# Optimization experiments

Hardware: AMD Instinct MI355X
Metric: run time of the kernel (lower is better)

Reference implementation:

```python
import jax, jax.numpy as jnp
import numpy as np

B, L, V, D, H, DK, NL, M = 4, 1024, 64, 256, 4, 64, 4, 20
FF = 4 * D
EPS = 1e-5


def _rel_table(seq_len, m):
    # abs(i-j), log-bucketed beyond m, clipped to [0, 2m] -> int indices [L, L]
    d = jnp.abs(jnp.arange(seq_len)[:, None] - jnp.arange(seq_len)[None, :]).astype(jnp.float32)
    d = jnp.where(d > m, m + jnp.log2(jnp.maximum(d - m, 1.0)), d)
    return jnp.clip(d, 0, 2 * m).astype(jnp.int32)


def _layer_norm(x, g, b):
    mu = jnp.mean(x, axis=-1, keepdims=True)
    var = jnp.mean(jnp.square(x - mu), axis=-1, keepdims=True)
    return (x - mu) * jax.lax.rsqrt(var + EPS) * g + b


def setup_inputs() -> dict:
    key = jax.random.key(0)
    ks = jax.random.split(key, 16)
    w = lambda i, shape: jax.random.normal(ks[i], shape, jnp.float32) * 0.05
    return {
        "x": jax.random.normal(ks[0], (B, L, V), jnp.float32),
        "emb": w(1, (V, D)),
        "Wq": w(2, (NL, D, H * DK)), "bq": jnp.zeros((NL, H * DK), jnp.float32),
        "Wk": w(3, (NL, D, H * DK)), "bk": jnp.zeros((NL, H * DK), jnp.float32),
        "Wv": w(4, (NL, D, H * DK)), "bv": jnp.zeros((NL, H * DK), jnp.float32),
        "Wo": w(5, (NL, H * DK, D)), "bo": jnp.zeros((NL, D), jnp.float32),
        "rel_k": 1.0 + w(6, (NL, 2 * M + 1, H)),  # multiplicative bias ~1
        "rel_b": w(7, (NL, 2 * M + 1, H)),
        "ln1_g": jnp.ones((NL, D), jnp.float32), "ln1_b": jnp.zeros((NL, D), jnp.float32),
        "W1": w(8, (NL, D, FF)), "b1": jnp.zeros((NL, FF), jnp.float32),
        "W2": w(9, (NL, FF, D)), "b2": jnp.zeros((NL, D), jnp.float32),
        "ln2_g": jnp.ones((NL, D), jnp.float32), "ln2_b": jnp.zeros((NL, D), jnp.float32),
    }


def reference(x, emb, Wq, bq, Wk, bk, Wv, bv, Wo, bo, rel_k, rel_b,
              ln1_g, ln1_b, W1, b1, W2, b2, ln2_g, ln2_b):
    h = x @ emb  # [B, L, D]  (dropout inactive: eval mode)
    table = _rel_table(L, M)  # [L, L] int32
    inv_sqrt_dk = jnp.float32(1.0 / np.sqrt(DK))
    attns = []
    for l in range(NL):
        q = (h @ Wq[l] + bq[l]).reshape(B, L, H, DK)
        k = (h @ Wk[l] + bk[l]).reshape(B, L, H, DK)
        v = (h @ Wv[l] + bv[l]).reshape(B, L, H, DK)
        scores = jnp.einsum('blhk,bmhk->bhlm', q, k) * inv_sqrt_dk
        # per-head relative-position bias (table symmetric, so axis order of L,L is immaterial)
        bias_k = jnp.transpose(rel_k[l][table], (2, 1, 0))  # [H, L, L]
        bias_b = jnp.transpose(rel_b[l][table], (2, 1, 0))  # [H, L, L]
        scores = scores * bias_k[None] + bias_b[None]
        attn = jax.nn.softmax(scores, axis=-1)  # attn dropout inactive (eval)
        attns.append(attn)
        out = jnp.einsum('bhlm,bmhk->blhk', attn, v).reshape(B, L, H * DK) @ Wo[l] + bo[l]
        # FeedForwardNetwork (note: source has NO residual connections)
        y = _layer_norm(out, ln1_g[l], ln1_b[l])
        y = jax.nn.gelu(y @ W1[l] + b1[l], approximate=False) @ W2[l] + b2[l]
        h = _layer_norm(y, ln2_g[l], ln2_b[l])
    avg_attn = jnp.mean(jnp.stack(attns, axis=0), axis=0)  # [B, H, L, L]
    return h.mean(axis=1), avg_attn
```

## Files before the change

kernel.cpp:

```cpp
#include <hip/hip_runtime.h>
#include <hip/hip_bf16.h>
#include <math.h>

#define Bn 4
#define Ln 1024
#define Vn 64
#define Dn 256
#define Hn 4
#define DKn 64
#define NLn 4
#define Mn 20
#define FFn 1024
#define NTOK (Bn * Ln)
#define QKVW 768
#define LOG2E 1.4426950408889634f
#define PELEMS (Bn * Hn * Ln * Ln)

typedef __attribute__((ext_vector_type(8))) short bf16x8;
typedef __attribute__((ext_vector_type(4))) float f32x4;

__device__ __forceinline__ ushort f2b(float f) {
    uint u = __float_as_uint(f);
    u += 0x7fff + ((u >> 16) & 1);
    return (ushort)(u >> 16);
}
__device__ __forceinline__ float b2f(ushort u) {
    return __uint_as_float(((uint)u) << 16);
}

__global__ __launch_bounds__(256) void embed_k(const float* __restrict__ X,
                                               const float* __restrict__ E,
                                               ushort* __restrict__ Hb) {
    __shared__ float xs[Vn];
    int n = blockIdx.x, d = threadIdx.x;
    if (threadIdx.x < Vn) xs[threadIdx.x] = X[n * Vn + threadIdx.x];
    __syncthreads();
    float s = 0.f;
#pragma unroll
    for (int v = 0; v < Vn; ++v) s += xs[v] * E[v * Dn + d];
    Hb[(size_t)n * Dn + d] = f2b(s);
}

__global__ __launch_bounds__(256) void relbias_k(const float* __restrict__ rk,
                                                 const float* __restrict__ rb,
                                                 float* __restrict__ bkT,
                                                 float* __restrict__ bbT) {
    int tid = blockIdx.x * 256 + threadIdx.x;
    int dist = tid & 1023;
    int hh = (tid >> 10) & 3;
    int l = tid >> 12;
    float dd = (float)dist;
    if (dist > Mn) dd = (float)Mn + log2f((float)(dist - Mn));
    if (dd > 2.0f * Mn) dd = 2.0f * Mn;
    int idx = (int)dd;
    bkT[tid] = rk[(l * (2 * Mn + 1) + idx) * Hn + hh] * 0.125f * LOG2E;
    bbT[tid] = rb[(l * (2 * Mn + 1) + idx) * Hn + hh] * LOG2E;
}

__global__ __launch_bounds__(256) void prep_bias(const float* __restrict__ bq,
                                                 const float* __restrict__ bk,
                                                 const float* __restrict__ bv,
                                                 float* __restrict__ bqkv) {
    int idx = blockIdx.x * 256 + threadIdx.x;
    int l = idx / QKVW, r = idx - l * QKVW;
    float v;
    if (r < 256)      v = bq[l * 256 + r];
    else if (r < 512) v = bk[l * 256 + r - 256];
    else              v = bv[l * 256 + r - 512];
    bqkv[idx] = v;
}

__global__ __launch_bounds__(256) void transpose_cvt(
    const float* __restrict__ src, ushort* __restrict__ dst,
    int R, int C, int srcLS, int dstLS) {
    __shared__ float s[32][33];
    src += (size_t)blockIdx.z * srcLS;
    dst += (size_t)blockIdx.z * dstLS;
    int r0 = blockIdx.y * 32, c0 = blockIdx.x * 32;
    int tx = threadIdx.x & 31, ty = threadIdx.x >> 5;
#pragma unroll
    for (int ii = 0; ii < 4; ++ii)
        s[ty + 8 * ii][tx] = src[(size_t)(r0 + ty + 8 * ii) * C + c0 + tx];
    __syncthreads();
#pragma unroll
    for (int ii = 0; ii < 4; ++ii)
        dst[(size_t)(c0 + ty + 8 * ii) * R + r0 + tx] = f2b(s[tx][ty + 8 * ii]);
}

#define GST 72
#define GEMM_KK_MFMA(KK)                                                      \
    {                                                                         \
        bf16x8 a0 = *(const bf16x8*)&As[(wm * 32 + l15) * GST + (KK)*32 + lg * 8];      \
        bf16x8 a1 = *(const bf16x8*)&As[(wm * 32 + 16 + l15) * GST + (KK)*32 + lg * 8]; \
        bf16x8 b0 = *(const bf16x8*)&Bs[(wn * 32 + l15) * GST + (KK)*32 + lg * 8];      \
        bf16x8 b1 = *(const bf16x8*)&Bs[(wn * 32 + 16 + l15) * GST + (KK)*32 + lg * 8]; \
        acc[0][0] = __builtin_amdgcn_mfma_f32_16x16x32_bf16(a0, b0, acc[0][0], 0, 0, 0); \
        acc[0][1] = __builtin_amdgcn_mfma_f32_16x16x32_bf16(a0, b1, acc[0][1], 0, 0, 0); \
        acc[1][0] = __builtin_amdgcn_mfma_f32_16x16x32_bf16(a1, b0, acc[1][0], 0, 0, 0); \
        acc[1][1] = __builtin_amdgcn_mfma_f32_16x16x32_bf16(a1, b1, acc[1][1], 0, 0, 0); \
    }

template <int LNA>
__global__ __launch_bounds__(256) void gemm_mfma(
    const ushort* __restrict__ A, const ushort* __restrict__ Bt,
    const float* __restrict__ bias, ushort* __restrict__ C,
    int M, int N, int K, int act,
    const float* __restrict__ lng, const float* __restrict__ lnb,
    ushort* __restrict__ Vt_out) {
    __shared__ __align__(16) ushort As[64 * GST];
    __shared__ __align__(16) ushort Bs[64 * GST];
    __shared__ float gl[256];
    __shared__ float bl[256];
    int t = threadIdx.x;
    int lane = t & 63, w = t >> 6;
    int wm = w >> 1, wn = w & 1;
    int l15 = lane & 15, lg = lane >> 4;
    int mBase = blockIdx.y * 64, nBase = blockIdx.x * 64;
    int lrow = t >> 2, lkc = (t & 3) * 16;
    const ushort* Ap = A + (size_t)(mBase + lrow) * K + lkc;
    const ushort* Bp = Bt + (size_t)(nBase + lrow) * K + lkc;
    f32x4 acc[2][2] = {};

    if constexpr (LNA) {
        uint4 areg[8];
        float s = 0.f;
#pragma unroll
        for (int kc = 0; kc < 4; ++kc)
#pragma unroll
            for (int h = 0; h < 2; ++h) {
                areg[kc * 2 + h] = *(const uint4*)(Ap + kc * 64 + h * 8);
                const ushort* e = (const ushort*)&areg[kc * 2 + h];
#pragma unroll
                for (int q = 0; q < 8; ++q) s += b2f(e[q]);
            }
        s += __shfl_xor(s, 1, 64);
        s += __shfl_xor(s, 2, 64);
        float mu = s * (1.0f / 256.0f);
        float vv = 0.f;
#pragma unroll
        for (int kc = 0; kc < 8; ++kc) {
            const ushort* e = (const ushort*)&areg[kc];
#pragma unroll
            for (int q = 0; q < 8; ++q) {
                float d = b2f(e[q]) - mu;
                vv += d * d;
            }
        }
        vv += __shfl_xor(vv, 1, 64);
        vv += __shfl_xor(vv, 2, 64);
        float rs = rsqrtf(vv * (1.0f / 256.0f) + 1e-5f);
        gl[t] = lng[t];
        bl[t] = lnb[t];
        __syncthreads();
#pragma unroll
        for (int kc = 0; kc < 4; ++kc) {
            uint4 bv0 = *(const uint4*)(Bp + kc * 64);
            uint4 bv1 = *(const uint4*)(Bp + kc * 64 + 8);
            __syncthreads();
#pragma unroll
            for (int h = 0; h < 2; ++h) {
                const ushort* e = (const ushort*)&areg[kc * 2 + h];
                ushort outv[8];
#pragma unroll
                for (int q = 0; q < 8; ++q) {
                    int col = kc * 64 + lkc + h * 8 + q;
                    outv[q] = f2b((b2f(e[q]) - mu) * rs * gl[col] + bl[col]);
                }
                *(uint4*)&As[lrow * GST + lkc + h * 8] = *(const uint4*)outv;
            }
            *(uint4*)&Bs[lrow * GST + lkc] = bv0;
            *(uint4*)&Bs[lrow * GST + lkc + 8] = bv1;
            __syncthreads();
            GEMM_KK_MFMA(0)
            GEMM_KK_MFMA(1)
        }
    } else {
        for (int k0 = 0; k0 < K; k0 += 64) {
            uint4 av0 = *(const uint4*)(Ap + k0);
            uint4 av1 = *(const uint4*)(Ap + k0 + 8);
            uint4 bv0 = *(const uint4*)(Bp + k0);
            uint4 bv1 = *(const uint4*)(Bp + k0 + 8);
            __syncthreads();
            *(uint4*)&As[lrow * GST + lkc] = av0;
            *(uint4*)&As[lrow * GST + lkc + 8] = av1;
            *(uint4*)&Bs[lrow * GST + lkc] = bv0;
            *(uint4*)&Bs[lrow * GST + lkc + 8] = bv1;
            __syncthreads();
            GEMM_KK_MFMA(0)
            GEMM_KK_MFMA(1)
        }
    }
    if (Vt_out != nullptr && nBase >= 512) {
#pragma unroll
        for (int ni = 0; ni < 2; ++ni) {
            int col = nBase + wn * 32 + ni * 16 + l15;
            float bc = bias[col];
            int d = col - 512;
#pragma unroll
            for (int mi = 0; mi < 2; ++mi) {
                int rb = mBase + wm * 32 + mi * 16 + lg * 4;
                int bb_ = rb >> 10, i_ = rb & 1023;
                size_t vb = ((size_t)(bb_ * 4 + (d >> 6)) * 64 + (d & 63)) * Ln + i_;
                ushort o4[4];
#pragma unroll
                for (int j = 0; j < 4; ++j) o4[j] = f2b(acc[mi][ni][j] + bc);
                *(ushort4*)&Vt_out[vb] = *(const ushort4*)o4;
            }
        }
        return;
    }
#pragma unroll
    for (int ni = 0; ni < 2; ++ni) {
        int col = nBase + wn * 32 + ni * 16 + l15;
        float bc = bias[col];
#pragma unroll
        for (int mi = 0; mi < 2; ++mi) {
            int rb = mBase + wm * 32 + mi * 16 + lg * 4;
#pragma unroll
            for (int j = 0; j < 4; ++j) {
                float v = acc[mi][ni][j] + bc;
                if (act) v = v * 0.5f * (1.0f + erff(v * 0.7071067811865475f));
                C[(size_t)(rb + j) * N + col] = f2b(v);
            }
        }
    }
}

#define G2ST 72
template <int LNA, int SPLITK>
__global__ __launch_bounds__(512) void gemm128(
    const ushort* __restrict__ A, const ushort* __restrict__ Bt,
    const float* __restrict__ bias, ushort* __restrict__ C,
    float* __restrict__ Cpart,
    int M, int N, int K, int act,
    const float* __restrict__ lng, const float* __restrict__ lnb,
    ushort* __restrict__ Vt_out) {
    __shared__ __align__(16) ushort As[128 * G2ST];
    __shared__ __align__(16) ushort Bs[128 * G2ST];
    __shared__ float gl[256];
    __shared__ float bl[256];
    int t = threadIdx.x;
    int lane = t & 63, w = t >> 6;
    int wm = w >> 2, wn = w & 3;
    int l15 = lane & 15, lg = lane >> 4;
    int mBase = blockIdx.y * 128, nBase = blockIdx.x * 128;
    int srow = t >> 2, skof = (t & 3) * 16;
    int kbeg = (SPLITK > 1) ? blockIdx.z * 256 : 0;
    const ushort* Ap = A + (size_t)(mBase + srow) * K + kbeg + skof;
    const ushort* Bp = Bt + (size_t)(nBase + srow) * K + kbeg + skof;
    f32x4 acc[4][2] = {};

    float mu = 0.f, rs = 0.f;
    uint4 areg[8];
    if constexpr (LNA) {
        float s = 0.f;
#pragma unroll
        for (int kc = 0; kc < 4; ++kc)
#pragma unroll
            for (int h = 0; h < 2; ++h) {
                areg[kc * 2 + h] = *(const uint4*)(Ap + kc * 64 + h * 8);
                const ushort* e = (const ushort*)&areg[kc * 2 + h];
#pragma unroll
                for (int z = 0; z < 8; ++z) s += b2f(e[z]);
            }
        s += __shfl_xor(s, 1, 64);
        s += __shfl_xor(s, 2, 64);
        mu = s * (1.0f / 256.0f);
        float vv = 0.f;
#pragma unroll
        for (int q = 0; q < 8; ++q) {
            const ushort* e = (const ushort*)&areg[q];
#pragma unroll
            for (int z = 0; z < 8; ++z) {
                float d = b2f(e[z]) - mu;
                vv += d * d;
            }
        }
        vv += __shfl_xor(vv, 1, 64);
        vv += __shfl_xor(vv, 2, 64);
        rs = rsqrtf(vv * (1.0f / 256.0f) + 1e-5f);
        if (t < 256) {
            gl[t] = lng[t];
            bl[t] = lnb[t];
        }
    }

#pragma unroll
    for (int kc = 0; kc < 4; ++kc) {
        uint4 av0, av1, bv0, bv1;
        if constexpr (!LNA) {
            av0 = *(const uint4*)(Ap + kc * 64);
            av1 = *(const uint4*)(Ap + kc * 64 + 8);
        }
        bv0 = *(const uint4*)(Bp + kc * 64);
        bv1 = *(const uint4*)(Bp + kc * 64 + 8);
        __syncthreads();
        if constexpr (LNA) {
#pragma unroll
            for (int h = 0; h < 2; ++h) {
                const ushort* e = (const ushort*)&areg[kc * 2 + h];
                ushort outv[8];
#pragma unroll
                for (int z = 0; z < 8; ++z) {
                    int col = kc * 64 + skof + h * 8 + z;
                    outv[z] = f2b((b2f(e[z]) - mu) * rs * gl[col] + bl[col]);
                }
                *(uint4*)&As[srow * G2ST + skof + h * 8] = *(const uint4*)outv;
            }
        } else {
            *(uint4*)&As[srow * G2ST + skof] = av0;
            *(uint4*)&As[srow * G2ST + skof + 8] = av1;
        }
        *(uint4*)&Bs[srow * G2ST + skof] = bv0;
        *(uint4*)&Bs[srow * G2ST + skof + 8] = bv1;
        __syncthreads();
#pragma unroll
        for (int kk = 0; kk < 2; ++kk) {
            bf16x8 af[4], bfr[2];
#pragma unroll
            for (int mi = 0; mi < 4; ++mi)
                af[mi] = *(const bf16x8*)&As[(wm * 64 + mi * 16 + l15) * G2ST + kk * 32 + lg * 8];
#pragma unroll
            for (int ni = 0; ni < 2; ++ni)
                bfr[ni] = *(const bf16x8*)&Bs[(wn * 32 + ni * 16 + l15) * G2ST + kk * 32 + lg * 8];
#pragma unroll
            for (int mi = 0; mi < 4; ++mi)
#pragma unroll
                for (int ni = 0; ni < 2; ++ni)
                    acc[mi][ni] = __builtin_amdgcn_mfma_f32_16x16x32_bf16(
                        af[mi], bfr[ni], acc[mi][ni], 0, 0, 0);
        }
    }

    if (Vt_out != nullptr && nBase >= 512) {
#pragma unroll
        for (int ni = 0; ni < 2; ++ni) {
            int col = nBase + wn * 32 + ni * 16 + l15;
            float bc = bias[col];
            int d = col - 512;
#pragma unroll
            for (int mi = 0; mi < 4; ++mi) {
                int rb = mBase + wm * 64 + mi * 16 + lg * 4;
                int bb_ = rb >> 10, i_ = rb & 1023;
                size_t vb = ((size_t)(bb_ * 4 + (d >> 6)) * 64 + (d & 63)) * Ln + i_;
                ushort o4[4];
#pragma unroll
                for (int j = 0; j < 4; ++j) o4[j] = f2b(acc[mi][ni][j] + bc);
                *(ushort4*)&Vt_out[vb] = *(const ushort4*)o4;
            }
        }
        return;
    }
    if constexpr (SPLITK > 1) {
#pragma unroll
        for (int ni = 0; ni < 2; ++ni) {
            int col = nBase + wn * 32 + ni * 16 + l15;
#pragma unroll
            for (int mi = 0; mi < 4; ++mi) {
                int rb = mBase + wm * 64 + mi * 16 + lg * 4;
#pragma unroll
                for (int j = 0; j < 4; ++j)
                    Cpart[((size_t)blockIdx.z * M + rb + j) * N + col] = acc[mi][ni][j];
            }
        }
        return;
    }
#pragma unroll
    for (int ni = 0; ni < 2; ++ni) {
        int col = nBase + wn * 32 + ni * 16 + l15;
        float bc = bias[col];
#pragma unroll
        for (int mi = 0; mi < 4; ++mi) {
            int rb = mBase + wm * 64 + mi * 16 + lg * 4;
#pragma unroll
            for (int j = 0; j < 4; ++j) {
                float v = acc[mi][ni][j] + bc;
                if (act) v = v * 0.5f * (1.0f + erff(v * 0.7071067811865475f));
                C[(size_t)(rb + j) * N + col] = f2b(v);
            }
        }
    }
}

__global__ __launch_bounds__(256) void combine_k(const float* __restrict__ part,
                                                 const float* __restrict__ bias,
                                                 ushort* __restrict__ C) {
    size_t e = ((size_t)blockIdx.x * 256 + threadIdx.x) * 4;
    const size_t MN = (size_t)NTOK * Dn;
    float4 s = *(const float4*)&bias[(int)(e & 255)];
#pragma unroll
    for (int z = 0; z < 4; ++z) {
        float4 p = *(const float4*)&part[z * MN + e];
        s.x += p.x; s.y += p.y; s.z += p.z; s.w += p.w;
    }
    ushort4 o;
    o.x = f2b(s.x); o.y = f2b(s.y); o.z = f2b(s.z); o.w = f2b(s.w);
    *(ushort4*)&C[e] = o;
}

#define PWST 40
#define NW 8
template <int MODE>
__global__ __launch_bounds__(512) void attn_fused(
    const ushort* __restrict__ qkv, const ushort* __restrict__ Vt,
    const float* __restrict__ bkTab, const float* __restrict__ bbTab,
    ushort* __restrict__ ctx, float* __restrict__ avg,
    ushort* __restrict__ Pout, int first) {
    __shared__ float bk_l[Ln];
    __shared__ float bb_l[Ln];
    __shared__ __align__(16) char uni[20480];
    __shared__ float mm[NW][16];
    __shared__ float ll[NW][16];

    int t = threadIdx.x;
    int lane = t & 63, w = t >> 6;
    int wn = w & 3, wc = w >> 2;
    int l15 = lane & 15, lg = lane >> 4;

    ushort* pwh = (ushort*)&uni[w * 2560];
    ushort* pwl = (ushort*)&uni[w * 2560 + 1280];

    int bid = blockIdx.x;
    int xcd = bid & 7, sub = bid >> 3;
    int bh = xcd * 2 + (sub >> 6);
    int q = sub & 63;
    int b = bh >> 2, hh = bh & 3;
    int i0 = q * 16;

#pragma unroll
    for (int ii = 0; ii < 2; ++ii) {
        bk_l[t + 512 * ii] = bkTab[hh * Ln + t + 512 * ii];
        bb_l[t + 512 * ii] = bbTab[hh * Ln + t + 512 * ii];
    }
    __syncthreads();

    bf16x8 qa0, qa1;
    {
        const ushort* qp = qkv + (size_t)(b * Ln + i0 + l15) * QKVW + hh * DKn;
        qa0 = *(const bf16x8*)(qp + lg * 8);
        qa1 = *(const bf16x8*)(qp + 32 + lg * 8);
    }

    const ushort* kbase = qkv + (size_t)(b * Ln) * QKVW + Dn + hh * DKn;

    f32x4 sv[8];
    float m[4] = {-1e30f, -1e30f, -1e30f, -1e30f};
#pragma unroll
    for (int cl = 0; cl < 8; ++cl) {
        int c = wc * 8 + cl;
        const ushort* kp = kbase + (size_t)(c * 64 + wn * 16 + l15) * QKVW;
        bf16x8 k0 = *(const bf16x8*)(kp + lg * 8);
        bf16x8 k1 = *(const bf16x8*)(kp + 32 + lg * 8);
        f32x4 acc = {};
        acc = __builtin_amdgcn_mfma_f32_16x16x32_bf16(qa0, k0, acc, 0, 0, 0);
        acc = __builtin_amdgcn_mfma_f32_16x16x32_bf16(qa1, k1, acc, 0, 0, 0);
        int j = c * 64 + wn * 16 + l15;
#pragma unroll
        for (int r = 0; r < 4; ++r) {
            int i = i0 + lg * 4 + r;
            int dist = (i > j) ? (i - j) : (j - i);
            float s = acc[r] * bk_l[dist] + bb_l[dist];
            sv[cl][r] = s;
            m[r] = fmaxf(m[r], s);
        }
    }
#pragma unroll
    for (int mask = 1; mask < 16; mask <<= 1)
#pragma unroll
        for (int r = 0; r < 4; ++r) m[r] = fmaxf(m[r], __shfl_xor(m[r], mask, 64));
    if (l15 == 0)
#pragma unroll
        for (int r = 0; r < 4; ++r) mm[w][lg * 4 + r] = m[r];
    __syncthreads();
#pragma unroll
    for (int r = 0; r < 4; ++r) {
        int row = lg * 4 + r;
        float m0 = fmaxf(fmaxf(mm[0][row], mm[1][row]), fmaxf(mm[2][row], mm[3][row]));
        float m1 = fmaxf(fmaxf(mm[4][row], mm[5][row]), fmaxf(mm[6][row], mm[7][row]));
        m[r] = fmaxf(m0, m1);
    }
    float lsum[4] = {0.f, 0.f, 0.f, 0.f};
#pragma unroll
    for (int cl = 0; cl < 8; ++cl)
#pragma unroll
        for (int r = 0; r < 4; ++r) {
            float p = exp2f(sv[cl][r] - m[r]);
            sv[cl][r] = p;
            lsum[r] += p;
        }
#pragma unroll
    for (int mask = 1; mask < 16; mask <<= 1)
#pragma unroll
        for (int r = 0; r < 4; ++r) lsum[r] += __shfl_xor(lsum[r], mask, 64);
    if (l15 == 0)
#pragma unroll
        for (int r = 0; r < 4; ++r) ll[w][lg * 4 + r] = lsum[r];
    __syncthreads();
    float invl[4];
#pragma unroll
    for (int r = 0; r < 4; ++r) {
        int row = lg * 4 + r;
        invl[r] = 1.0f / (ll[0][row] + ll[1][row] + ll[2][row] + ll[3][row] +
                          ll[4][row] + ll[5][row] + ll[6][row] + ll[7][row]);
    }

    const ushort* vbase = Vt + (size_t)bh * DKn * Ln;
    float* avgrow = avg + ((size_t)bh * Ln + i0) * Ln;
    int iw = lane >> 2, jq = lane & 3;
    f32x4 acco[4] = {};
#pragma unroll
    for (int p = 0; p < 4; ++p) {
        const int c0 = wc * 8 + 2 * p, c1 = c0 + 1;
        float aold[2][4];
        if (MODE == 0 && !first) {
#pragma unroll
            for (int cc = 0; cc < 2; ++cc)
#pragma unroll
                for (int r = 0; r < 4; ++r)
                    aold[cc][r] = avgrow[(size_t)(lg * 4 + r) * Ln +
                                         (c0 + cc) * 64 + wn * 16 + l15];
        }
#pragma unroll
        for (int cc = 0; cc < 2; ++cc)
#pragma unroll
            for (int r = 0; r < 4; ++r) {
                float pv = sv[2 * p + cc][r] * invl[r];
                sv[2 * p + cc][r] = pv;
                ushort ph = f2b(pv);
                int off = (lg * 4 + r) * PWST + cc * 16 + l15;
                pwh[off] = ph;
                pwl[off] = f2b(pv - b2f(ph));
            }
        int kcol = (lg < 2 ? c0 : c1) * 64 + wn * 16 + (lg & 1) * 8;
        bf16x8 va0 = *(const bf16x8*)(vbase + (size_t)(0 * 16 + l15) * Ln + kcol);
        bf16x8 va1 = *(const bf16x8*)(vbase + (size_t)(1 * 16 + l15) * Ln + kcol);
        bf16x8 va2 = *(const bf16x8*)(vbase + (size_t)(2 * 16 + l15) * Ln + kcol);
        bf16x8 va3 = *(const bf16x8*)(vbase + (size_t)(3 * 16 + l15) * Ln + kcol);
        bf16x8 pbh = *(const bf16x8*)&pwh[l15 * PWST + lg * 8];
        bf16x8 pbl = *(const bf16x8*)&pwl[l15 * PWST + lg * 8];
        acco[0] = __builtin_amdgcn_mfma_f32_16x16x32_bf16(va0, pbh, acco[0], 0, 0, 0);
        acco[1] = __builtin_amdgcn_mfma_f32_16x16x32_bf16(va1, pbh, acco[1], 0, 0, 0);
        acco[2] = __builtin_amdgcn_mfma_f32_16x16x32_bf16(va2, pbh, acco[2], 0, 0, 0);
        acco[3] = __builtin_amdgcn_mfma_f32_16x16x32_bf16(va3, pbh, acco[3], 0, 0, 0);
        acco[0] = __builtin_amdgcn_mfma_f32_16x16x32_bf16(va0, pbl, acco[0], 0, 0, 0);
        acco[1] = __builtin_amdgcn_mfma_f32_16x16x32_bf16(va1, pbl, acco[1], 0, 0, 0);
        acco[2] = __builtin_amdgcn_mfma_f32_16x16x32_bf16(va2, pbl, acco[2], 0, 0, 0);
        acco[3] = __builtin_amdgcn_mfma_f32_16x16x32_bf16(va3, pbl, acco[3], 0, 0, 0);
        if (MODE == 0) {
#pragma unroll
            for (int cc = 0; cc < 2; ++cc)
#pragma unroll
                for (int r = 0; r < 4; ++r) {
                    float v = 0.25f * sv[2 * p + cc][r];
                    if (!first) v += aold[cc][r];
                    avgrow[(size_t)(lg * 4 + r) * Ln + (c0 + cc) * 64 + wn * 16 + l15] = v;
                }
        } else if (MODE == 1) {
            size_t tb = ((((size_t)bid * 8 + w) * 4 + p) * 2) * 256 + (size_t)lane * 4;
            ushort4 ph0 = *(const ushort4*)&pwh[iw * PWST + 0 * 16 + jq * 4];
            ushort4 ph1 = *(const ushort4*)&pwh[iw * PWST + 1 * 16 + jq * 4];
            *(ushort4*)&Pout[tb] = ph0;
            *(ushort4*)&Pout[tb + 256] = ph1;
        } else {
#pragma unroll
            for (int cc = 0; cc < 2; ++cc) {
                int c = c0 + cc;
                size_t tb = ((((size_t)bid * 8 + w) * 4 + p) * 2 + cc) * 256 +
                            (size_t)lane * 4;
                ushort4 p0 = *(const ushort4*)&Pout[tb];
                ushort4 p1 = *(const ushort4*)&Pout[(size_t)PELEMS + tb];
                ushort4 p2 = *(const ushort4*)&Pout[(size_t)2 * PELEMS + tb];
                ushort4 p3 = *(const ushort4*)&pwh[iw * PWST + cc * 16 + jq * 4];
                const ushort* q0 = (const ushort*)&p0;
                const ushort* q1 = (const ushort*)&p1;
                const ushort* q2 = (const ushort*)&p2;
                const ushort* q3 = (const ushort*)&p3;
                size_t base = ((size_t)(bh * Ln) + i0 + iw) * Ln +
                              c * 64 + wn * 16 + jq * 4;
                float4 o;
                float* op_ = (float*)&o;
#pragma unroll
                for (int k = 0; k < 4; ++k)
                    op_[k] = 0.25f * (b2f(q0[k]) + b2f(q1[k]) + b2f(q2[k]) + b2f(q3[k]));
                *(float4*)&avg[base] = o;
            }
        }
    }

    __syncthreads();
    {
        float* op = (float*)&uni[wn * 4096];
        if (wc == 1) {
#pragma unroll
            for (int dg = 0; dg < 4; ++dg)
#pragma unroll
                for (int r = 0; r < 4; ++r)
                    op[(dg * 16 + lg * 4 + r) * 16 + l15] = acco[dg][r];
        }
    }
    __syncthreads();
    {
        float* op = (float*)&uni[wn * 4096];
        if (wc == 0) {
#pragma unroll
            for (int dg = 0; dg < 4; ++dg)
#pragma unroll
                for (int r = 0; r < 4; ++r)
                    op[(dg * 16 + lg * 4 + r) * 16 + l15] += acco[dg][r];
        }
    }
    __syncthreads();
#pragma unroll
    for (int k = 0; k < 2; ++k) {
        int idx = t + 512 * k;
        float v = ((const float*)&uni[0])[idx] + ((const float*)&uni[4096])[idx] +
                  ((const float*)&uni[8192])[idx] + ((const float*)&uni[12288])[idx];
        int dd = idx >> 4, ii = idx & 15;
        ctx[(size_t)(b * Ln + i0 + ii) * Dn + hh * DKn + dd] = f2b(v);
    }
}

__global__ __launch_bounds__(256) void layernorm_k(const ushort* __restrict__ X,
                                                   const float* __restrict__ g,
                                                   const float* __restrict__ bta,
                                                   ushort* __restrict__ Y) {
    int w = threadIdx.x >> 6, lane = threadIdx.x & 63;
    int row = blockIdx.x * 4 + w;
    const ushort* xr = X + (size_t)row * Dn;
    float x[4];
#pragma unroll
    for (int ii = 0; ii < 4; ++ii) x[ii] = b2f(xr[lane + 64 * ii]);
    float s = x[0] + x[1] + x[2] + x[3];
#pragma unroll
    for (int m = 1; m < 64; m <<= 1) s += __shfl_xor(s, m, 64);
    float mu = s * (1.0f / 256.0f);
    float vs = 0.f;
#pragma unroll
    for (int ii = 0; ii < 4; ++ii) {
        float d = x[ii] - mu;
        vs += d * d;
    }
#pragma unroll
    for (int m = 1; m < 64; m <<= 1) vs += __shfl_xor(vs, m, 64);
    float rs = rsqrtf(vs * (1.0f / 256.0f) + 1e-5f);
#pragma unroll
    for (int ii = 0; ii < 4; ++ii) {
        int d = lane + 64 * ii;
        Y[(size_t)row * Dn + d] = f2b((x[ii] - mu) * rs * g[d] + bta[d]);
    }
}

__global__ __launch_bounds__(256) void mean_part_k(const ushort* __restrict__ Hb,
                                                   float* __restrict__ part) {
    int blk = blockIdx.x;
    int b = blk >> 4, g = blk & 15;
    int d = threadIdx.x;
    float s = 0.f;
#pragma unroll
    for (int r = 0; r < 64; ++r)
        s += b2f(Hb[(size_t)(b * Ln + g * 64 + r) * Dn + d]);
    part[(size_t)blk * Dn + d] = s;
}
__global__ __launch_bounds__(256) void mean_final_k(const float* __restrict__ part,
                                                    float* __restrict__ out) {
    int b = blockIdx.x, d = threadIdx.x;
    float s = 0.f;
#pragma unroll
    for (int g = 0; g < 16; ++g) s += part[(size_t)(b * 16 + g) * Dn + d];
    out[b * Dn + d] = s * (1.0f / (float)Ln);
}

extern "C" void kernel_launch(void* const* d_in, const int* in_sizes, int n_in,
                              void* d_out, int out_size, void* d_ws, size_t ws_size,
                              hipStream_t stream) {
    const float* x    = (const float*)d_in[0];
    const float* emb  = (const float*)d_in[1];
    const float* Wq   = (const float*)d_in[2];
    const float* bq   = (const float*)d_in[3];
    const float* Wk   = (const float*)d_in[4];
    const float* bk   = (const float*)d_in[5];
    const float* Wv   = (const float*)d_in[6];
    const float* bv   = (const float*)d_in[7];
    const float* Wo   = (const float*)d_in[8];
    const float* bo   = (const float*)d_in[9];
    const float* rk   = (const float*)d_in[10];
    const float* rb   = (const float*)d_in[11];
    const float* ln1g = (const float*)d_in[12];
    const float* ln1b = (const float*)d_in[13];
    const float* W1   = (const float*)d_in[14];
    const float* b1   = (const float*)d_in[15];
    const float* W2   = (const float*)d_in[16];
    const float* b2   = (const float*)d_in[17];
    const float* ln2g = (const float*)d_in[18];
    const float* ln2b = (const float*)d_in[19];

    float* out = (float*)d_out;
    float* avg = out + Bn * Dn;

    char* ws = (char*)d_ws;
    const size_t MB = 1024 * 1024;
    ushort* hb   = (ushort*)(ws);
    ushort* qkvb = (ushort*)(ws + 2 * MB);
    ushort* ctxb = (ushort*)(ws + 8 * MB);
    ushort* t1   = (ushort*)(ws + 10 * MB);
    ushort* ffb  = (ushort*)(ws + 12 * MB);
    ushort* qkvT = (ushort*)(ws + 20 * MB);
    ushort* WoT  = (ushort*)(ws + 22 * MB);
    ushort* W1T  = (ushort*)(ws + 23 * MB);
    ushort* W2T  = (ushort*)(ws + 25 * MB);
    float*  bqkv = (float*)(ws + 27 * MB);
    float*  bkT  = (float*)(ws + 27 * MB + 65536);
    float*  bbT  = (float*)(ws + 27 * MB + 131072);
    ushort* Vt   = (ushort*)(ws + 30 * MB);
    float*  mpart= (float*)(ws + 33 * MB);
    ushort* Pbuf = (ushort*)(ws + 36 * MB);
    float*  fpart= (float*)(ws + 132 * MB);

    const size_t need = 132 * MB + (size_t)4 * NTOK * Dn * sizeof(float);
    const bool fancy = (ws_size >= need);

    embed_k<<<NTOK, 256, 0, stream>>>(x, emb, hb);
    relbias_k<<<64, 256, 0, stream>>>(rk, rb, bkT, bbT);
    prep_bias<<<12, 256, 0, stream>>>(bq, bk, bv, bqkv);

    dim3 t88(8, 8, NLn);
    transpose_cvt<<<t88, 256, 0, stream>>>(Wq, qkvT + 0,      256, 256, 65536, 196608);
    transpose_cvt<<<t88, 256, 0, stream>>>(Wk, qkvT + 65536,  256, 256, 65536, 196608);
    transpose_cvt<<<t88, 256, 0, stream>>>(Wv, qkvT + 131072, 256, 256, 65536, 196608);
    transpose_cvt<<<t88, 256, 0, stream>>>(Wo, WoT,           256, 256, 65536, 65536);
    transpose_cvt<<<dim3(32, 8, NLn), 256, 0, stream>>>(W1, W1T, 256, 1024, 262144, 262144);
    transpose_cvt<<<dim3(8, 32, NLn), 256, 0, stream>>>(W2, W2T, 1024, 256, 262144, 262144);

    for (int l = 0; l < NLn; ++l) {
        if (fancy) {
            if (l == 0) {
                gemm128<0, 1><<<dim3(6, 32), 512, 0, stream>>>(
                    hb, qkvT + (size_t)l * 196608, bqkv + l * QKVW, qkvb, nullptr,
                    NTOK, QKVW, Dn, 0, nullptr, nullptr, Vt);
            } else {
                gemm128<1, 1><<<dim3(6, 32), 512, 0, stream>>>(
                    hb, qkvT + (size_t)l * 196608, bqkv + l * QKVW, qkvb, nullptr,
                    NTOK, QKVW, Dn, 0, ln2g + (l - 1) * 256, ln2b + (l - 1) * 256, Vt);
            }
            if (l < 3) {
                attn_fused<1><<<1024, 512, 0, stream>>>(
                    qkvb, Vt, bkT + l * Hn * Ln, bbT + l * Hn * Ln, ctxb, avg,
                    Pbuf + (size_t)l * PELEMS, 0);
            } else {
                attn_fused<2><<<1024, 512, 0, stream>>>(
                    qkvb, Vt, bkT + l * Hn * Ln, bbT + l * Hn * Ln, ctxb, avg,
                    Pbuf, 0);
            }
            gemm_mfma<0><<<dim3(4, 64), 256, 0, stream>>>(
                ctxb, WoT + (size_t)l * 65536, bo + l * 256, t1,
                NTOK, Dn, Dn, 0, nullptr, nullptr, nullptr);
            gemm128<1, 1><<<dim3(8, 32), 512, 0, stream>>>(
                t1, W1T + (size_t)l * 262144, b1 + l * FFn, ffb, nullptr,
                NTOK, FFn, Dn, 1, ln1g + l * 256, ln1b + l * 256, nullptr);
            gemm128<0, 4><<<dim3(2, 32, 4), 512, 0, stream>>>(
                ffb, W2T + (size_t)l * 262144, nullptr, nullptr, fpart,
                NTOK, Dn, FFn, 0, nullptr, nullptr, nullptr);
            combine_k<<<1024, 256, 0, stream>>>(fpart, b2 + l * 256, hb);
        } else {
            if (l == 0) {
                gemm_mfma<0><<<dim3(12, 64), 256, 0, stream>>>(
                    hb, qkvT + (size_t)l * 196608, bqkv + l * QKVW, qkvb,
                    NTOK, QKVW, Dn, 0, nullptr, nullptr, Vt);
            } else {
                gemm_mfma<1><<<dim3(12, 64), 256, 0, stream>>>(
                    hb, qkvT + (size_t)l * 196608, bqkv + l * QKVW, qkvb,
                    NTOK, QKVW, Dn, 0, ln2g + (l - 1) * 256, ln2b + (l - 1) * 256, Vt);
            }
            attn_fused<0><<<1024, 512, 0, stream>>>(
                qkvb, Vt, bkT + l * Hn * Ln, bbT + l * Hn * Ln, ctxb, avg,
                (ushort*)Pbuf, (l == 0) ? 1 : 0);
            gemm_mfma<0><<<dim3(4, 64), 256, 0, stream>>>(
                ctxb, WoT + (size_t)l * 65536, bo + l * 256, t1,
                NTOK, Dn, Dn, 0, nullptr, nullptr, nullptr);
            gemm_mfma<1><<<dim3(16, 64), 256, 0, stream>>>(
                t1, W1T + (size_t)l * 262144, b1 + l * FFn, ffb,
                NTOK, FFn, Dn, 1, ln1g + l * 256, ln1b + l * 256, nullptr);
            gemm_mfma<0><<<dim3(4, 64), 256, 0, stream>>>(
                ffb, W2T + (size_t)l * 262144, b2 + l * 256, hb,
                NTOK, Dn, FFn, 0, nullptr, nullptr, nullptr);
        }
    }
    layernorm_k<<<NTOK / 4, 256, 0, stream>>>(
        hb, ln2g + 3 * 256, ln2b + 3 * 256, hb);
    mean_part_k<<<64, 256, 0, stream>>>(hb, mpart);
    mean_final_k<<<Bn, 256, 0, stream>>>(mpart, out);
}
```

Before: 380.5 us.

## Double attention block to 16 waves splitting key columns four ways

The fused attention kernel now launches 1024 threads (16 waves) per block instead of 512. Each wave handles 4 key column tiles instead of 8, which halves per-thread score registers and adds wave-level parallelism for latency hiding. Cross-wave max/sum reductions now span 16 entries, and the ctx reduction uses 8 partial slabs in shared memory, which adds extra LDS traffic and barrier cost. The P buffer indexing layout is changed consistently for the store and reload modes.

```diff
diff --git a/kernel.cpp b/kernel.cpp
--- a/kernel.cpp
+++ b/kernel.cpp
@@ -399,16 +399,16 @@
 }
 
 #define PWST 40
-#define NW 8
+#define NW 16
 template <int MODE>
-__global__ __launch_bounds__(512) void attn_fused(
+__global__ __launch_bounds__(1024, 8) void attn_fused(
     const ushort* __restrict__ qkv, const ushort* __restrict__ Vt,
     const float* __restrict__ bkTab, const float* __restrict__ bbTab,
     ushort* __restrict__ ctx, float* __restrict__ avg,
     ushort* __restrict__ Pout, int first) {
     __shared__ float bk_l[Ln];
     __shared__ float bb_l[Ln];
-    __shared__ __align__(16) char uni[20480];
+    __shared__ __align__(16) char uni[NW * 2560];
     __shared__ float mm[NW][16];
     __shared__ float ll[NW][16];
 
@@ -427,11 +427,8 @@
     int b = bh >> 2, hh = bh & 3;
     int i0 = q * 16;
 
-#pragma unroll
-    for (int ii = 0; ii < 2; ++ii) {
-        bk_l[t + 512 * ii] = bkTab[hh * Ln + t + 512 * ii];
-        bb_l[t + 512 * ii] = bbTab[hh * Ln + t + 512 * ii];
-    }
+    bk_l[t] = bkTab[hh * Ln + t];
+    bb_l[t] = bbTab[hh * Ln + t];
     __syncthreads();
 
     bf16x8 qa0, qa1;
@@ -443,11 +440,11 @@
 
     const ushort* kbase = qkv + (size_t)(b * Ln) * QKVW + Dn + hh * DKn;
 
-    f32x4 sv[8];
+    f32x4 sv[4];
     float m[4] = {-1e30f, -1e30f, -1e30f, -1e30f};
 #pragma unroll
-    for (int cl = 0; cl < 8; ++cl) {
-        int c = wc * 8 + cl;
+    for (int cl = 0; cl < 4; ++cl) {
+        int c = wc * 4 + cl;
         const ushort* kp = kbase + (size_t)(c * 64 + wn * 16 + l15) * QKVW;
         bf16x8 k0 = *(const bf16x8*)(kp + lg * 8);
         bf16x8 k1 = *(const bf16x8*)(kp + 32 + lg * 8);
@@ -475,13 +472,14 @@
 #pragma unroll
     for (int r = 0; r < 4; ++r) {
         int row = lg * 4 + r;
-        float m0 = fmaxf(fmaxf(mm[0][row], mm[1][row]), fmaxf(mm[2][row], mm[3][row]));
-        float m1 = fmaxf(fmaxf(mm[4][row], mm[5][row]), fmaxf(mm[6][row], mm[7][row]));
-        m[r] = fmaxf(m0, m1);
+        float mx = mm[0][row];
+#pragma unroll
+        for (int wv = 1; wv < NW; ++wv) mx = fmaxf(mx, mm[wv][row]);
+        m[r] = mx;
     }
     float lsum[4] = {0.f, 0.f, 0.f, 0.f};
 #pragma unroll
-    for (int cl = 0; cl < 8; ++cl)
+    for (int cl = 0; cl < 4; ++cl)
 #pragma unroll
         for (int r = 0; r < 4; ++r) {
             float p = exp2f(sv[cl][r] - m[r]);
@@ -500,8 +498,10 @@
 #pragma unroll
     for (int r = 0; r < 4; ++r) {
         int row = lg * 4 + r;
-        invl[r] = 1.0f / (ll[0][row] + ll[1][row] + ll[2][row] + ll[3][row] +
-                          ll[4][row] + ll[5][row] + ll[6][row] + ll[7][row]);
+        float sm = ll[0][row];
+#pragma unroll
+        for (int wv = 1; wv < NW; ++wv) sm += ll[wv][row];
+        invl[r] = 1.0f / sm;
     }
 
     const ushort* vbase = Vt + (size_t)bh * DKn * Ln;
@@ -509,8 +509,8 @@
     int iw = lane >> 2, jq = lane & 3;
     f32x4 acco[4] = {};
 #pragma unroll
-    for (int p = 0; p < 4; ++p) {
-        const int c0 = wc * 8 + 2 * p, c1 = c0 + 1;
+    for (int p = 0; p < 2; ++p) {
+        const int c0 = wc * 4 + 2 * p, c1 = c0 + 1;
         float aold[2][4];
         if (MODE == 0 && !first) {
 #pragma unroll
@@ -556,7 +556,7 @@
                     avgrow[(size_t)(lg * 4 + r) * Ln + (c0 + cc) * 64 + wn * 16 + l15] = v;
                 }
         } else if (MODE == 1) {
-            size_t tb = ((((size_t)bid * 8 + w) * 4 + p) * 2) * 256 + (size_t)lane * 4;
+            size_t tb = ((((size_t)bid * NW + w) * 2 + p) * 2) * 256 + (size_t)lane * 4;
             ushort4 ph0 = *(const ushort4*)&pwh[iw * PWST + 0 * 16 + jq * 4];
             ushort4 ph1 = *(const ushort4*)&pwh[iw * PWST + 1 * 16 + jq * 4];
             *(ushort4*)&Pout[tb] = ph0;
@@ -565,7 +565,7 @@
 #pragma unroll
             for (int cc = 0; cc < 2; ++cc) {
                 int c = c0 + cc;
-                size_t tb = ((((size_t)bid * 8 + w) * 4 + p) * 2 + cc) * 256 +
+                size_t tb = ((((size_t)bid * NW + w) * 2 + p) * 2 + cc) * 256 +
                             (size_t)lane * 4;
                 ushort4 p0 = *(const ushort4*)&Pout[tb];
                 ushort4 p1 = *(const ushort4*)&Pout[(size_t)PELEMS + tb];
@@ -589,8 +589,8 @@
 
     __syncthreads();
     {
-        float* op = (float*)&uni[wn * 4096];
-        if (wc == 1) {
+        float* op = (float*)&uni[(wn * 2 + (wc & 1)) * 4096];
+        if (wc >= 2) {
 #pragma unroll
             for (int dg = 0; dg < 4; ++dg)
 #pragma unroll
@@ -600,8 +600,8 @@
     }
     __syncthreads();
     {
-        float* op = (float*)&uni[wn * 4096];
-        if (wc == 0) {
+        float* op = (float*)&uni[(wn * 2 + (wc & 1)) * 4096];
+        if (wc < 2) {
 #pragma unroll
             for (int dg = 0; dg < 4; ++dg)
 #pragma unroll
@@ -610,11 +610,12 @@
         }
     }
     __syncthreads();
-#pragma unroll
-    for (int k = 0; k < 2; ++k) {
-        int idx = t + 512 * k;
-        float v = ((const float*)&uni[0])[idx] + ((const float*)&uni[4096])[idx] +
-                  ((const float*)&uni[8192])[idx] + ((const float*)&uni[12288])[idx];
+    {
+        int idx = t;
+        float v = 0.f;
+#pragma unroll
+        for (int rg = 0; rg < 8; ++rg)
+            v += ((const float*)&uni[rg * 4096])[idx];
         int dd = idx >> 4, ii = idx & 15;
         ctx[(size_t)(b * Ln + i0 + ii) * Dn + hh * DKn + dd] = f2b(v);
     }
@@ -743,11 +744,11 @@
                     NTOK, QKVW, Dn, 0, ln2g + (l - 1) * 256, ln2b + (l - 1) * 256, Vt);
             }
             if (l < 3) {
-                attn_fused<1><<<1024, 512, 0, stream>>>(
+                attn_fused<1><<<1024, 1024, 0, stream>>>(
                     qkvb, Vt, bkT + l * Hn * Ln, bbT + l * Hn * Ln, ctxb, avg,
                     Pbuf + (size_t)l * PELEMS, 0);
             } else {
-                attn_fused<2><<<1024, 512, 0, stream>>>(
+                attn_fused<2><<<1024, 1024, 0, stream>>>(
                     qkvb, Vt, bkT + l * Hn * Ln, bbT + l * Hn * Ln, ctxb, avg,
                     Pbuf, 0);
             }
@@ -771,7 +772,7 @@
                     hb, qkvT + (size_t)l * 196608, bqkv + l * QKVW, qkvb,
                     NTOK, QKVW, Dn, 0, ln2g + (l - 1) * 256, ln2b + (l - 1) * 256, Vt);
             }
-            attn_fused<0><<<1024, 512, 0, stream>>>(
+            attn_fused<0><<<1024, 1024, 0, stream>>>(
                 qkvb, Vt, bkT + l * Hn * Ln, bbT + l * Hn * Ln, ctxb, avg,
                 (ushort*)Pbuf, (l == 0) ? 1 : 0);
             gemm_mfma<0><<<dim3(4, 64), 256, 0, stream>>>(
```

New measurement: 409.9 us. 1.08x slower.
